# Kernel optimization log

Hardware: AMD Instinct MI355X
Metric: run time of the kernel (lower is better)

The kernel has to match this reference:

```python
import jax, jax.numpy as jnp
import numpy as np
import math

V, T, D_POI, D_OUT = 200000, 512, 256, 512
D_IN = D_POI + 4
D_HID = D_POI + 100


def setup_inputs() -> dict:
    key = jax.random.key(0)
    ks = jax.random.split(key, 12)
    s = 0.02
    return {
        "prev_poi_idx": jax.random.randint(ks[0], (T,), 0, V),
        "prev_time_frac": jax.random.uniform(ks[1], (T,), jnp.float32),
        "poi_final_emb": jax.random.normal(ks[2], (V, D_POI), jnp.float32),
        "poi_latlon_deg": jax.random.uniform(ks[3], (V, 2), jnp.float32) * 90.0,
        "ln_w": jnp.ones((D_IN,), jnp.float32),
        "ln_b": jnp.zeros((D_IN,), jnp.float32),
        "w1": jax.random.normal(ks[4], (D_IN, D_HID), jnp.float32) * s,
        "b1": jnp.zeros((D_HID,), jnp.float32),
        "w2": jax.random.normal(ks[5], (D_HID, D_POI), jnp.float32) * s,
        "b2": jnp.zeros((D_POI,), jnp.float32),
        "w_ih": jax.random.normal(ks[6], (3 * D_OUT, D_POI), jnp.float32) * s,
        "w_hh": jax.random.normal(ks[7], (3 * D_OUT, D_OUT), jnp.float32) * s,
        "b_ih": jnp.zeros((3 * D_OUT,), jnp.float32),
        "b_hh": jnp.zeros((3 * D_OUT,), jnp.float32),
        "q": jax.random.normal(ks[8], (D_OUT,), jnp.float32),
        "log_lam": jnp.array(0.0, jnp.float32),  # log(recency_lambda=1.0)
    }


def _haversine_km(lat1, lon1, lat2, lon2, eps=1e-12):
    dlat = (lat2 - lat1) * 0.5
    dlon = (lon2 - lon1) * 0.5
    a = jnp.sin(dlat) ** 2 + jnp.clip(jnp.cos(lat1), -1, 1) * jnp.clip(jnp.cos(lat2), -1, 1) * jnp.sin(dlon) ** 2
    c = 2.0 * jnp.arctan2(jnp.sqrt(jnp.clip(a, 0, 1)), jnp.sqrt(jnp.clip(1 - a, eps, 1)))
    return 6371.0088 * c


def _forward(prev_poi_idx, prev_time_frac, poi_final_emb, poi_latlon_deg,
             ln_w, ln_b, w1, b1, w2, b2, w_ih, w_hh, b_ih, b_hh, q, log_lam):
    Tn = prev_poi_idx.shape[0]
    poi_emb = poi_final_emb[prev_poi_idx]                       # (T, d_poi)
    t = jnp.clip(prev_time_frac, 0.0, 1.0)
    sin_t = jnp.sin(2.0 * math.pi * t)
    cos_t = jnp.cos(2.0 * math.pi * t)
    dif = jnp.mod(t[1:] - t[:-1], 1.0) * 24.0
    dt_h = jnp.concatenate([jnp.zeros((1,), t.dtype), dif])
    # _poi_radians is under no_grad in torch
    latlon = jax.lax.stop_gradient(poi_latlon_deg[prev_poi_idx])
    lat = jnp.deg2rad(jnp.clip(latlon[:, 0], -90, 90))
    lon = jnp.deg2rad(jnp.clip(latlon[:, 1], -180, 180))
    dd = _haversine_km(lat[:-1], lon[:-1], lat[1:], lon[1:])
    dd_km = jnp.concatenate([jnp.zeros((1,), dd.dtype), dd])
    feat = jnp.stack([sin_t, cos_t, jnp.log1p(dt_h), jnp.log1p(dd_km)], axis=-1)  # (T, 4)
    x = jnp.concatenate([poi_emb, feat], axis=-1)               # (T, d_poi+4)
    # fuse: LayerNorm -> Linear -> GELU -> (Dropout eval=id) -> Linear
    mu = jnp.mean(x, axis=-1, keepdims=True)
    var = jnp.mean((x - mu) ** 2, axis=-1, keepdims=True)
    x = (x - mu) * jax.lax.rsqrt(var + 1e-5) * ln_w + ln_b
    x = jax.nn.gelu(x @ w1 + b1, approximate=False) @ w2 + b2   # (T, d_poi)
    # GRU (single layer, unidirectional), torch gate order r,z,n
    gi_all = x @ w_ih.T + b_ih                                  # (T, 3H)
    def step(h, gi):
        gh = h @ w_hh.T + b_hh
        gi_r, gi_z, gi_n = jnp.split(gi, 3)
        gh_r, gh_z, gh_n = jnp.split(gh, 3)
        r = jax.nn.sigmoid(gi_r + gh_r)
        z = jax.nn.sigmoid(gi_z + gh_z)
        n = jnp.tanh(gi_n + r * gh_n)
        h_new = (1.0 - z) * n + z * h
        return h_new, h_new
    h0 = jnp.zeros((D_OUT,), x.dtype)
    _, hs = jax.lax.scan(step, h0, gi_all)                      # (T, d_out)
    D = hs.shape[-1]
    score = hs @ (q[:D] / jnp.sqrt(jnp.asarray(D, hs.dtype)))
    age = jnp.arange(Tn, dtype=hs.dtype)
    lam = jnp.maximum(jnp.exp(log_lam), 1e-4)
    score = score - lam * (Tn - 1 - age)
    attn = jax.nn.softmax(score, axis=0)
    summary = jnp.sum(attn[:, None] * hs, axis=0, keepdims=True)  # (1, d_out)
    return summary, attn


def reference(prev_poi_idx, prev_time_frac, poi_final_emb, poi_latlon_deg,
              ln_w, ln_b, w1, b1, w2, b2, w_ih, w_hh, b_ih, b_hh, q, log_lam):
    return _forward(prev_poi_idx, prev_time_frac, poi_final_emb, poi_latlon_deg,
                    ln_w, ln_b, w1, b1, w2, b2, w_ih, w_hh, b_ih, b_hh, q, log_lam)
```

## Files before the change

kernel.cpp:

```cpp
#include <hip/hip_runtime.h>
#include <hip/hip_cooperative_groups.h>
#include <math.h>

namespace cg = cooperative_groups;

#define TT 512
#define DPOI 256
#define DIN 260
#define DHID 356
#define DOUTD 512
#define G3 1536

#define GB 8
#define HU (DOUTD / GB)
#define NRR (3 * HU)
#define NPAY DOUTD

__global__ void ln_kernel(const int* __restrict__ idx, const float* __restrict__ timef,
                          const float* __restrict__ latlon, const float* __restrict__ emb,
                          const float* __restrict__ lnw, const float* __restrict__ lnb,
                          float* __restrict__ xn) {
    int t = blockIdx.x;
    int tid = threadIdx.x;
    int wave = tid >> 6, lane = tid & 63;

    float tv = fminf(fmaxf(timef[t], 0.f), 1.f);
    const float TWO_PI = 6.28318530717958647692f;
    float f0 = sinf(TWO_PI * tv);
    float f1 = cosf(TWO_PI * tv);
    float f2 = 0.f, f3 = 0.f;
    if (t > 0) {
        float tp = fminf(fmaxf(timef[t - 1], 0.f), 1.f);
        float d = tv - tp;
        d = d - floorf(d);
        f2 = log1pf(d * 24.f);
        int i0 = idx[t - 1], i1 = idx[t];
        float la0 = latlon[2 * (size_t)i0], lo0 = latlon[2 * (size_t)i0 + 1];
        float la1 = latlon[2 * (size_t)i1], lo1 = latlon[2 * (size_t)i1 + 1];
        const float D2R = 0.01745329251994329577f;
        float lat1 = fminf(fmaxf(la0, -90.f), 90.f) * D2R;
        float lon1 = fminf(fmaxf(lo0, -180.f), 180.f) * D2R;
        float lat2 = fminf(fmaxf(la1, -90.f), 90.f) * D2R;
        float lon2 = fminf(fmaxf(lo1, -180.f), 180.f) * D2R;
        float dlat = (lat2 - lat1) * 0.5f, dlon = (lon2 - lon1) * 0.5f;
        float sdlat = sinf(dlat), sdlon = sinf(dlon);
        float a = sdlat * sdlat +
                  fminf(fmaxf(cosf(lat1), -1.f), 1.f) * fminf(fmaxf(cosf(lat2), -1.f), 1.f) * sdlon * sdlon;
        float aa = fminf(fmaxf(a, 0.f), 1.f);
        float bb = fminf(fmaxf(1.f - a, 1e-12f), 1.f);
        float cc = 2.f * atan2f(sqrtf(aa), sqrtf(bb));
        f3 = log1pf(6371.0088f * cc);
    }
    float fv = (tid == 0) ? f0 : (tid == 1) ? f1 : (tid == 2) ? f2 : f3;

    const float* row = emb + (size_t)idx[t] * DPOI;
    float v0 = row[tid];
    float v1 = (tid < 4) ? fv : 0.f;

    __shared__ float red[4];
    __shared__ float mu_s, rs_s;

    float s = v0 + v1;
    for (int o = 32; o; o >>= 1) s += __shfl_down(s, o, 64);
    if (lane == 0) red[wave] = s;
    __syncthreads();
    if (tid == 0) mu_s = (red[0] + red[1] + red[2] + red[3]) * (1.f / 260.f);
    __syncthreads();
    float mu = mu_s;
    float d0 = v0 - mu;
    float d1 = (tid < 4) ? (v1 - mu) : 0.f;
    float sq = d0 * d0 + d1 * d1;
    for (int o = 32; o; o >>= 1) sq += __shfl_down(sq, o, 64);
    __syncthreads();
    if (lane == 0) red[wave] = sq;
    __syncthreads();
    if (tid == 0) {
        float var = (red[0] + red[1] + red[2] + red[3]) * (1.f / 260.f);
        rs_s = rsqrtf(var + 1e-5f);
    }
    __syncthreads();
    float rs = rs_s;
    xn[t * DIN + tid] = d0 * rs * lnw[tid] + lnb[tid];
    if (tid < 4)
        xn[t * DIN + 256 + tid] = d1 * rs * lnw[256 + tid] + lnb[256 + tid];
}

__global__ void mlp1_kernel(const float* __restrict__ xn, const float* __restrict__ w1,
                            const float* __restrict__ b1, float* __restrict__ h1) {
    int t = blockIdx.x, j = threadIdx.x;
    __shared__ float xl[DIN];
    for (int k = threadIdx.x; k < DIN; k += blockDim.x) xl[k] = xn[t * DIN + k];
    __syncthreads();
    if (j < DHID) {
        float acc = b1[j];
        #pragma unroll 4
        for (int k = 0; k < DIN; ++k) acc = fmaf(xl[k], w1[k * DHID + j], acc);
        float g = 0.5f * acc * (1.f + erff(acc * 0.70710678118654752440f));
        h1[t * DHID + j] = g;
    }
}

__global__ void mlp2_kernel(const float* __restrict__ h1, const float* __restrict__ w2,
                            const float* __restrict__ b2, float* __restrict__ x2) {
    int t = blockIdx.x, j = threadIdx.x;
    __shared__ float xl[DHID];
    for (int k = threadIdx.x; k < DHID; k += blockDim.x) xl[k] = h1[t * DHID + k];
    __syncthreads();
    float acc = b2[j];
    #pragma unroll 4
    for (int k = 0; k < DHID; ++k) acc = fmaf(xl[k], w2[k * DPOI + j], acc);
    x2[t * DPOI + j] = acc;
}

__global__ void gi_kernel(const float* __restrict__ x2, const float* __restrict__ wih,
                          const float* __restrict__ bih, float* __restrict__ gi,
                          uint4* __restrict__ hcz) {
    int t = blockIdx.x;
    int tid = threadIdx.x;
    int wave = tid >> 6, lane = tid & 63;
    uint4 z; z.x = 0u; z.y = 0u; z.z = 0u; z.w = 0u;
    hcz[(size_t)t * 256 + tid] = z;
    float4 xv = ((const float4*)(x2 + (size_t)t * DPOI))[lane];
    for (int r = wave; r < G3; r += 4) {
        float4 wv = ((const float4*)(wih + (size_t)r * DPOI))[lane];
        float s = xv.x * wv.x + xv.y * wv.y + xv.z * wv.z + xv.w * wv.w;
        for (int o = 32; o; o >>= 1) s += __shfl_down(s, o, 64);
        if (lane == 0) gi[(size_t)t * G3 + r] = s + bih[r];
    }
}

__global__ __launch_bounds__(1024)
void gru_fused_kernel(const float* __restrict__ gi, const float* __restrict__ whh,
                      const float* __restrict__ bhh, float* __restrict__ hs,
                      unsigned long long* __restrict__ hcomm,
                      const float* __restrict__ q, const float* __restrict__ log_lam,
                      float* __restrict__ out) {
    __shared__ float hprev[DOUTD];
    __shared__ float gsum[NRR];
    __shared__ float sc[TT];
    __shared__ float at[TT];
    __shared__ float red[8];
    __shared__ float red2[8];
    __shared__ float denom_s, mx_s;

    int b = blockIdx.x;
    int tid = threadIdx.x;
    int wave = tid >> 6, lane = tid & 63;
    int jbase = b * HU;
    int g4 = lane >> 4, l4 = lane & 15;
    int rr0 = wave * 12 + g4 * 3;

    float4 wf0[8], wf1[8], wf2[8];
    float bl0, bl1, bl2;
    {
        int r0 = rr0, r1 = rr0 + 1, r2 = rr0 + 2;
        const float4* p0 = (const float4*)(whh + (size_t)((r0 >> 6) * DOUTD + jbase + (r0 & 63)) * DOUTD);
        const float4* p1 = (const float4*)(whh + (size_t)((r1 >> 6) * DOUTD + jbase + (r1 & 63)) * DOUTD);
        const float4* p2 = (const float4*)(whh + (size_t)((r2 >> 6) * DOUTD + jbase + (r2 & 63)) * DOUTD);
        #pragma unroll
        for (int m = 0; m < 8; ++m) {
            wf0[m] = p0[m * 16 + l4];
            wf1[m] = p1[m * 16 + l4];
            wf2[m] = p2[m * 16 + l4];
        }
        bl0 = bhh[(r0 >> 6) * DOUTD + jbase + (r0 & 63)];
        bl1 = bhh[(r1 >> 6) * DOUTD + jbase + (r1 & 63)];
        bl2 = bhh[(r2 >> 6) * DOUTD + jbase + (r2 & 63)];
    }
    if (tid < DOUTD) hprev[tid] = 0.f;
    __syncthreads();

    const float4* hp4 = (const float4*)hprev;
    long budget = 2L * 1000 * 1000;
    float dj = (float)tid * 1e-6f;

    float gir = 0.f, giz = 0.f, gin = 0.f, hreg = 0.f;
    if (tid < HU) {
        int j = jbase + tid;
        gir = gi[j];
        giz = gi[DOUTD + j];
        gin = gi[2 * DOUTD + j];
    }

    for (int s = 0; s < TT; ++s) {
        if (s > 0) {
            if (tid >= 256 && tid < 768) {
                int u = tid - 256;
                bool own = (u >> 6) == b;
                const unsigned long long* ap = hcomm + (size_t)(s - 1) * NPAY + u;
                unsigned long long p = 0;
                bool ok = own;
                unsigned tagw = (unsigned)s;
                while (!__all(ok)) {
                    if (!ok) {
                        p = __hip_atomic_load(ap, __ATOMIC_RELAXED,
                                              __HIP_MEMORY_SCOPE_AGENT);
                        ok = ((unsigned)p == tagw);
                    }
                    float x = dj;
                    #pragma unroll
                    for (int zz = 0; zz < 8; ++zz) x = fmaf(x, 1.0000001f, 1e-7f);
                    dj = x;
                    if (--budget < 0) break;
                }
                if (!own) hprev[u] = __uint_as_float((unsigned)(p >> 32));
            }
            __syncthreads();
        }

        float a0 = 0.f, a1 = 0.f, a2 = 0.f;
        #pragma unroll
        for (int m = 0; m < 8; ++m) {
            float4 h4 = hp4[m * 16 + l4];
            a0 = fmaf(wf0[m].x, h4.x, a0); a0 = fmaf(wf0[m].y, h4.y, a0);
            a0 = fmaf(wf0[m].z, h4.z, a0); a0 = fmaf(wf0[m].w, h4.w, a0);
            a1 = fmaf(wf1[m].x, h4.x, a1); a1 = fmaf(wf1[m].y, h4.y, a1);
            a1 = fmaf(wf1[m].z, h4.z, a1); a1 = fmaf(wf1[m].w, h4.w, a1);
            a2 = fmaf(wf2[m].x, h4.x, a2); a2 = fmaf(wf2[m].y, h4.y, a2);
            a2 = fmaf(wf2[m].z, h4.z, a2); a2 = fmaf(wf2[m].w, h4.w, a2);
        }
        #pragma unroll
        for (int o = 1; o < 16; o <<= 1) {
            a0 += __shfl_xor(a0, o, 64);
            a1 += __shfl_xor(a1, o, 64);
            a2 += __shfl_xor(a2, o, 64);
        }
        if (l4 == 0) {
            gsum[rr0]     = a0 + bl0;
            gsum[rr0 + 1] = a1 + bl1;
            gsum[rr0 + 2] = a2 + bl2;
        }
        __syncthreads();

        if (tid < HU) {
            float gr  = gir + gsum[tid];
            float gz  = giz + gsum[HU + tid];
            float ghn = gsum[2 * HU + tid];
            float r = __builtin_amdgcn_rcpf(1.f + __expf(-gr));
            float z = __builtin_amdgcn_rcpf(1.f + __expf(-gz));
            float xt = gin + r * ghn;
            float n = 1.f - 2.f * __builtin_amdgcn_rcpf(__expf(2.f * xt) + 1.f);
            float hn = (1.f - z) * n + z * hreg;
            hreg = hn;
            unsigned ub = __float_as_uint(hn);
            ub += 0x7fffu + ((ub >> 16) & 1u);
            unsigned long long pay = ((unsigned long long)(ub & 0xffff0000u) << 32) |
                                     (unsigned)(s + 1);
            __hip_atomic_store(&hcomm[(size_t)s * NPAY + jbase + tid], pay,
                               __ATOMIC_RELAXED, __HIP_MEMORY_SCOPE_AGENT);
            int j = jbase + tid;
            hs[(size_t)s * DOUTD + j] = hn;
            hprev[j] = hn;
            if (s + 1 < TT) {
                const float* gn = gi + (size_t)(s + 1) * G3;
                gir = gn[j]; giz = gn[DOUTD + j]; gin = gn[2 * DOUTD + j];
            }
        }
    }

    asm volatile("" :: "v"(dj));

    cg::this_grid().sync();
    if (b != 0) return;

    const float qscale = 0.04419417382415921757f;
    for (int r = wave; r < TT; r += 16) {
        float acc = 0.f;
        #pragma unroll
        for (int m = 0; m < 8; ++m) {
            int k = lane + 64 * m;
            acc = fmaf(hs[(size_t)r * DOUTD + k], q[k], acc);
        }
        for (int o = 32; o; o >>= 1) acc += __shfl_down(acc, o, 64);
        if (lane == 0) sc[r] = acc * qscale;
    }
    __syncthreads();
    float lam = fmaxf(expf(log_lam[0]), 1e-4f);
    float s_i = (tid < TT) ? (sc[tid] - lam * (float)(TT - 1 - tid)) : -1e30f;

    float mval = s_i;
    for (int o = 32; o; o >>= 1) mval = fmaxf(mval, __shfl_down(mval, o, 64));
    if (lane == 0 && wave < 8) red[wave] = mval;
    __syncthreads();
    if (tid == 0) {
        float mm = red[0];
        for (int i = 1; i < 8; ++i) mm = fmaxf(mm, red[i]);
        mx_s = mm;
    }
    __syncthreads();
    float e = (tid < TT) ? expf(s_i - mx_s) : 0.f;
    float ssum = e;
    for (int o = 32; o; o >>= 1) ssum += __shfl_down(ssum, o, 64);
    if (lane == 0 && wave < 8) red2[wave] = ssum;
    __syncthreads();
    if (tid == 0) {
        float dsum = 0.f;
        for (int i = 0; i < 8; ++i) dsum += red2[i];
        denom_s = dsum;
    }
    __syncthreads();
    if (tid < TT) {
        float attn = e / denom_s;
        out[DOUTD + tid] = attn;
        at[tid] = attn;
    }
    __syncthreads();
    if (tid < TT) {
        float acc = 0.f;
        for (int i = 0; i < TT; ++i) acc = fmaf(at[i], hs[(size_t)i * DOUTD + tid], acc);
        out[tid] = acc;
    }
}

extern "C" void kernel_launch(void* const* d_in, const int* in_sizes, int n_in,
                              void* d_out, int out_size, void* d_ws, size_t ws_size,
                              hipStream_t stream) {
    const int*   idx    = (const int*)d_in[0];
    const float* timef  = (const float*)d_in[1];
    const float* emb    = (const float*)d_in[2];
    const float* latlon = (const float*)d_in[3];
    const float* lnw    = (const float*)d_in[4];
    const float* lnb    = (const float*)d_in[5];
    const float* w1     = (const float*)d_in[6];
    const float* b1     = (const float*)d_in[7];
    const float* w2     = (const float*)d_in[8];
    const float* b2     = (const float*)d_in[9];
    const float* wih    = (const float*)d_in[10];
    const float* whh    = (const float*)d_in[11];
    const float* bih    = (const float*)d_in[12];
    const float* bhh    = (const float*)d_in[13];
    const float* q      = (const float*)d_in[14];
    const float* loglam = (const float*)d_in[15];
    float* out = (float*)d_out;

    unsigned long long* hcomm = (unsigned long long*)d_ws;
    float* xn   = (float*)(hcomm + (size_t)TT * NPAY);
    float* h1   = xn + TT * DIN;
    float* x2   = h1 + TT * DHID;
    float* gi   = x2 + TT * DPOI;
    float* hs   = gi + (size_t)TT * G3;

    ln_kernel<<<TT, 256, 0, stream>>>(idx, timef, latlon, emb, lnw, lnb, xn);
    mlp1_kernel<<<TT, 384, 0, stream>>>(xn, w1, b1, h1);
    mlp2_kernel<<<TT, 256, 0, stream>>>(h1, w2, b2, x2);
    gi_kernel<<<TT, 256, 0, stream>>>(x2, wih, bih, gi, (uint4*)hcomm);

    void* gru_args[] = { (void*)&gi, (void*)&whh, (void*)&bhh, (void*)&hs,
                         (void*)&hcomm, (void*)&q, (void*)&loglam, (void*)&out };
    hipLaunchCooperativeKernel((void*)gru_fused_kernel, dim3(GB), dim3(1024),
                               gru_args, 0, stream);
}
```

Before: 1.849 ms.

## Fuse pre-GRU kernels, pack bf16 handoff into 32-bit words, split attention out

Merges the layernorm, two MLP layers and the input-gate projection into one kernel per timestep, with intermediates kept in shared memory, which removes three launches and their global round-trips. The GRU cross-block exchange now packs the bf16 hidden value and a 16-bit step tag into one 32-bit word. Waiting blocks poll it with hand-written inline assembly that keeps two loads in flight and uses a small retry budget. The cooperative launch and grid sync are replaced by ordinary launches plus a separate attention kernel. This relies on all 8 blocks being co-resident without a cooperative launch, and the short budget risks stale hidden values if a producer block lags.

```diff
diff --git a/kernel.cpp b/kernel.cpp
--- a/kernel.cpp
+++ b/kernel.cpp
@@ -1,8 +1,5 @@
 #include <hip/hip_runtime.h>
-#include <hip/hip_cooperative_groups.h>
 #include <math.h>
-
-namespace cg = cooperative_groups;
 
 #define TT 512
 #define DPOI 256
@@ -16,13 +13,25 @@
 #define NRR (3 * HU)
 #define NPAY DOUTD
 
-__global__ void ln_kernel(const int* __restrict__ idx, const float* __restrict__ timef,
-                          const float* __restrict__ latlon, const float* __restrict__ emb,
-                          const float* __restrict__ lnw, const float* __restrict__ lnb,
-                          float* __restrict__ xn) {
+__global__ __launch_bounds__(512)
+void pre_kernel(const int* __restrict__ idx, const float* __restrict__ timef,
+                const float* __restrict__ latlon, const float* __restrict__ emb,
+                const float* __restrict__ lnw, const float* __restrict__ lnb,
+                const float* __restrict__ w1, const float* __restrict__ b1,
+                const float* __restrict__ w2, const float* __restrict__ b2,
+                const float* __restrict__ wih, const float* __restrict__ bih,
+                float* __restrict__ gi, unsigned* __restrict__ hcz) {
     int t = blockIdx.x;
     int tid = threadIdx.x;
     int wave = tid >> 6, lane = tid & 63;
+
+    __shared__ float xl[DIN];
+    __shared__ float h1l[DHID];
+    __shared__ alignas(16) float x2l[DPOI];
+    __shared__ float red[8];
+    __shared__ float mu_s, rs_s;
+
+    hcz[(size_t)t * 512 + tid] = 0u;
 
     float tv = fminf(fmaxf(timef[t], 0.f), 1.f);
     const float TWO_PI = 6.28318530717958647692f;
@@ -53,21 +62,21 @@
     }
     float fv = (tid == 0) ? f0 : (tid == 1) ? f1 : (tid == 2) ? f2 : f3;
 
-    const float* row = emb + (size_t)idx[t] * DPOI;
-    float v0 = row[tid];
+    float v0 = (tid < 256) ? emb[(size_t)idx[t] * DPOI + tid] : 0.f;
     float v1 = (tid < 4) ? fv : 0.f;
-
-    __shared__ float red[4];
-    __shared__ float mu_s, rs_s;
 
     float s = v0 + v1;
     for (int o = 32; o; o >>= 1) s += __shfl_down(s, o, 64);
     if (lane == 0) red[wave] = s;
     __syncthreads();
-    if (tid == 0) mu_s = (red[0] + red[1] + red[2] + red[3]) * (1.f / 260.f);
+    if (tid == 0) {
+        float mm = 0.f;
+        for (int i = 0; i < 8; ++i) mm += red[i];
+        mu_s = mm * (1.f / 260.f);
+    }
     __syncthreads();
     float mu = mu_s;
-    float d0 = v0 - mu;
+    float d0 = (tid < 256) ? (v0 - mu) : 0.f;
     float d1 = (tid < 4) ? (v1 - mu) : 0.f;
     float sq = d0 * d0 + d1 * d1;
     for (int o = 32; o; o >>= 1) sq += __shfl_down(sq, o, 64);
@@ -75,73 +84,47 @@
     if (lane == 0) red[wave] = sq;
     __syncthreads();
     if (tid == 0) {
-        float var = (red[0] + red[1] + red[2] + red[3]) * (1.f / 260.f);
-        rs_s = rsqrtf(var + 1e-5f);
+        float vv = 0.f;
+        for (int i = 0; i < 8; ++i) vv += red[i];
+        rs_s = rsqrtf(vv * (1.f / 260.f) + 1e-5f);
     }
     __syncthreads();
     float rs = rs_s;
-    xn[t * DIN + tid] = d0 * rs * lnw[tid] + lnb[tid];
-    if (tid < 4)
-        xn[t * DIN + 256 + tid] = d1 * rs * lnw[256 + tid] + lnb[256 + tid];
+    if (tid < 256) xl[tid] = d0 * rs * lnw[tid] + lnb[tid];
+    if (tid < 4)   xl[256 + tid] = d1 * rs * lnw[256 + tid] + lnb[256 + tid];
+    __syncthreads();
+
+    if (tid < DHID) {
+        float acc = b1[tid];
+        #pragma unroll 4
+        for (int k = 0; k < DIN; ++k) acc = fmaf(xl[k], w1[k * DHID + tid], acc);
+        h1l[tid] = 0.5f * acc * (1.f + erff(acc * 0.70710678118654752440f));
+    }
+    __syncthreads();
+
+    if (tid < DPOI) {
+        float acc = b2[tid];
+        #pragma unroll 4
+        for (int k = 0; k < DHID; ++k) acc = fmaf(h1l[k], w2[k * DPOI + tid], acc);
+        x2l[tid] = acc;
+    }
+    __syncthreads();
+
+    float4 xv = ((const float4*)x2l)[lane];
+    for (int r = wave; r < G3; r += 8) {
+        float4 wv = ((const float4*)(wih + (size_t)r * DPOI))[lane];
+        float sd = xv.x * wv.x + xv.y * wv.y + xv.z * wv.z + xv.w * wv.w;
+        for (int o = 32; o; o >>= 1) sd += __shfl_down(sd, o, 64);
+        if (lane == 0) gi[(size_t)t * G3 + r] = sd + bih[r];
+    }
 }
 
-__global__ void mlp1_kernel(const float* __restrict__ xn, const float* __restrict__ w1,
-                            const float* __restrict__ b1, float* __restrict__ h1) {
-    int t = blockIdx.x, j = threadIdx.x;
-    __shared__ float xl[DIN];
-    for (int k = threadIdx.x; k < DIN; k += blockDim.x) xl[k] = xn[t * DIN + k];
-    __syncthreads();
-    if (j < DHID) {
-        float acc = b1[j];
-        #pragma unroll 4
-        for (int k = 0; k < DIN; ++k) acc = fmaf(xl[k], w1[k * DHID + j], acc);
-        float g = 0.5f * acc * (1.f + erff(acc * 0.70710678118654752440f));
-        h1[t * DHID + j] = g;
-    }
-}
-
-__global__ void mlp2_kernel(const float* __restrict__ h1, const float* __restrict__ w2,
-                            const float* __restrict__ b2, float* __restrict__ x2) {
-    int t = blockIdx.x, j = threadIdx.x;
-    __shared__ float xl[DHID];
-    for (int k = threadIdx.x; k < DHID; k += blockDim.x) xl[k] = h1[t * DHID + k];
-    __syncthreads();
-    float acc = b2[j];
-    #pragma unroll 4
-    for (int k = 0; k < DHID; ++k) acc = fmaf(xl[k], w2[k * DPOI + j], acc);
-    x2[t * DPOI + j] = acc;
-}
-
-__global__ void gi_kernel(const float* __restrict__ x2, const float* __restrict__ wih,
-                          const float* __restrict__ bih, float* __restrict__ gi,
-                          uint4* __restrict__ hcz) {
-    int t = blockIdx.x;
-    int tid = threadIdx.x;
-    int wave = tid >> 6, lane = tid & 63;
-    uint4 z; z.x = 0u; z.y = 0u; z.z = 0u; z.w = 0u;
-    hcz[(size_t)t * 256 + tid] = z;
-    float4 xv = ((const float4*)(x2 + (size_t)t * DPOI))[lane];
-    for (int r = wave; r < G3; r += 4) {
-        float4 wv = ((const float4*)(wih + (size_t)r * DPOI))[lane];
-        float s = xv.x * wv.x + xv.y * wv.y + xv.z * wv.z + xv.w * wv.w;
-        for (int o = 32; o; o >>= 1) s += __shfl_down(s, o, 64);
-        if (lane == 0) gi[(size_t)t * G3 + r] = s + bih[r];
-    }
-}
-
 __global__ __launch_bounds__(1024)
-void gru_fused_kernel(const float* __restrict__ gi, const float* __restrict__ whh,
-                      const float* __restrict__ bhh, float* __restrict__ hs,
-                      unsigned long long* __restrict__ hcomm,
-                      const float* __restrict__ q, const float* __restrict__ log_lam,
-                      float* __restrict__ out) {
-    __shared__ float hprev[DOUTD];
+void gru_kernel(const float* __restrict__ gi, const float* __restrict__ whh,
+                const float* __restrict__ bhh, float* __restrict__ hs,
+                unsigned* __restrict__ hcomm) {
+    __shared__ alignas(16) float hprev[DOUTD];
     __shared__ float gsum[NRR];
-    __shared__ float sc[TT];
-    __shared__ float at[TT];
-    __shared__ float red[8];
-    __shared__ float red2[8];
-    __shared__ float denom_s, mx_s;
 
     int b = blockIdx.x;
     int tid = threadIdx.x;
@@ -171,8 +154,7 @@
     __syncthreads();
 
     const float4* hp4 = (const float4*)hprev;
-    long budget = 2L * 1000 * 1000;
-    float dj = (float)tid * 1e-6f;
+    long budget = 3000;
 
     float gir = 0.f, giz = 0.f, gin = 0.f, hreg = 0.f;
     if (tid < HU) {
@@ -183,29 +165,50 @@
     }
 
     for (int s = 0; s < TT; ++s) {
+        unsigned pa = 0, pb = 0;
         if (s > 0) {
-            if (tid >= 256 && tid < 768) {
-                int u = tid - 256;
-                bool own = (u >> 6) == b;
-                const unsigned long long* ap = hcomm + (size_t)(s - 1) * NPAY + u;
-                unsigned long long p = 0;
-                bool ok = own;
-                unsigned tagw = (unsigned)s;
-                while (!__all(ok)) {
-                    if (!ok) {
-                        p = __hip_atomic_load(ap, __ATOMIC_RELAXED,
-                                              __HIP_MEMORY_SCOPE_AGENT);
-                        ok = ((unsigned)p == tagw);
-                    }
-                    float x = dj;
-                    #pragma unroll
-                    for (int zz = 0; zz < 8; ++zz) x = fmaf(x, 1.0000001f, 1e-7f);
-                    dj = x;
-                    if (--budget < 0) break;
-                }
-                if (!own) hprev[u] = __uint_as_float((unsigned)(p >> 32));
+            if (wave >= 4 && wave < 12 && (wave - 4) != b) {
+                int u = ((wave - 4) << 6) + lane;
+                const unsigned* ap = hcomm + (size_t)(s - 1) * NPAY + u;
+                unsigned tag = (unsigned)s & 0xffffu;
+                asm volatile("global_load_dword %0, %1, off sc0 sc1"
+                             : "=v"(pa) : "v"(ap) : "memory");
+                float xx = (float)(lane + 1) * 1e-6f;
+                #pragma unroll
+                for (int q = 0; q < 256; ++q) xx = fmaf(xx, 1.0000002f, 1.1920929e-7f);
+                asm volatile("global_load_dword %0, %1, off sc0 sc1"
+                             : "=v"(pb) : "v"(ap), "v"(xx) : "memory");
+                do {
+                    unsigned tmp; int scnt;
+                    asm volatile(
+                        "s_movk_i32 %[cnt], 64\n\t"
+                        "1:\n\t"
+                        "s_waitcnt vmcnt(1)\n\t"
+                        "v_and_b32 %[t], 0xffff, %[pa]\n\t"
+                        "v_cmp_ne_u32 vcc, %[tag], %[t]\n\t"
+                        "s_cbranch_vccz 9f\n\t"
+                        "global_load_dword %[pa], %[ptr], off sc0 sc1\n\t"
+                        "s_waitcnt vmcnt(1)\n\t"
+                        "v_and_b32 %[t], 0xffff, %[pb]\n\t"
+                        "v_cmp_ne_u32 vcc, %[tag], %[t]\n\t"
+                        "s_cbranch_vccz 8f\n\t"
+                        "global_load_dword %[pb], %[ptr], off sc0 sc1\n\t"
+                        "s_sub_u32 %[cnt], %[cnt], 1\n\t"
+                        "s_cmp_lg_u32 %[cnt], 0\n\t"
+                        "s_cbranch_scc1 1b\n\t"
+                        "s_branch 9f\n\t"
+                        "8:\n\t"
+                        "v_mov_b32 %[pa], %[pb]\n\t"
+                        "9:\n\t"
+                        : [pa]"+v"(pa), [pb]"+v"(pb), [t]"=&v"(tmp), [cnt]"=&s"(scnt)
+                        : [ptr]"v"(ap), [tag]"s"(tag)
+                        : "vcc", "scc", "memory");
+                    if ((pa & 0xffffu) == tag) break;
+                } while (--budget > 0);
+                hprev[u] = __uint_as_float(pa & 0xffff0000u);
             }
             __syncthreads();
+            asm volatile("" :: "v"(pa), "v"(pb));
         }
 
         float a0 = 0.f, a1 = 0.f, a2 = 0.f;
@@ -244,8 +247,7 @@
             hreg = hn;
             unsigned ub = __float_as_uint(hn);
             ub += 0x7fffu + ((ub >> 16) & 1u);
-            unsigned long long pay = ((unsigned long long)(ub & 0xffff0000u) << 32) |
-                                     (unsigned)(s + 1);
+            unsigned pay = (ub & 0xffff0000u) | ((unsigned)(s + 1) & 0xffffu);
             __hip_atomic_store(&hcomm[(size_t)s * NPAY + jbase + tid], pay,
                                __ATOMIC_RELAXED, __HIP_MEMORY_SCOPE_AGENT);
             int j = jbase + tid;
@@ -257,14 +259,20 @@
             }
         }
     }
-
-    asm volatile("" :: "v"(dj));
-
-    cg::this_grid().sync();
-    if (b != 0) return;
+}
+
+__global__ void attn_kernel(const float* __restrict__ hs, const float* __restrict__ q,
+                            const float* __restrict__ log_lam, float* __restrict__ out) {
+    int tid = threadIdx.x;
+    int wave = tid >> 6, lane = tid & 63;
+    __shared__ float sc[TT];
+    __shared__ float at[TT];
+    __shared__ float red[8];
+    __shared__ float red2[8];
+    __shared__ float denom_s, mx_s;
 
     const float qscale = 0.04419417382415921757f;
-    for (int r = wave; r < TT; r += 16) {
+    for (int r = wave; r < TT; r += 8) {
         float acc = 0.f;
         #pragma unroll
         for (int m = 0; m < 8; ++m) {
@@ -276,11 +284,11 @@
     }
     __syncthreads();
     float lam = fmaxf(expf(log_lam[0]), 1e-4f);
-    float s_i = (tid < TT) ? (sc[tid] - lam * (float)(TT - 1 - tid)) : -1e30f;
+    float s_i = sc[tid] - lam * (float)(TT - 1 - tid);
 
     float mval = s_i;
     for (int o = 32; o; o >>= 1) mval = fmaxf(mval, __shfl_down(mval, o, 64));
-    if (lane == 0 && wave < 8) red[wave] = mval;
+    if (lane == 0) red[wave] = mval;
     __syncthreads();
     if (tid == 0) {
         float mm = red[0];
@@ -288,10 +296,10 @@
         mx_s = mm;
     }
     __syncthreads();
-    float e = (tid < TT) ? expf(s_i - mx_s) : 0.f;
+    float e = expf(s_i - mx_s);
     float ssum = e;
     for (int o = 32; o; o >>= 1) ssum += __shfl_down(ssum, o, 64);
-    if (lane == 0 && wave < 8) red2[wave] = ssum;
+    if (lane == 0) red2[wave] = ssum;
     __syncthreads();
     if (tid == 0) {
         float dsum = 0.f;
@@ -299,17 +307,13 @@
         denom_s = dsum;
     }
     __syncthreads();
-    if (tid < TT) {
-        float attn = e / denom_s;
-        out[DOUTD + tid] = attn;
-        at[tid] = attn;
-    }
-    __syncthreads();
-    if (tid < TT) {
-        float acc = 0.f;
-        for (int i = 0; i < TT; ++i) acc = fmaf(at[i], hs[(size_t)i * DOUTD + tid], acc);
-        out[tid] = acc;
-    }
+    float attn = e / denom_s;
+    out[DOUTD + tid] = attn;
+    at[tid] = attn;
+    __syncthreads();
+    float acc = 0.f;
+    for (int i = 0; i < TT; ++i) acc = fmaf(at[i], hs[(size_t)i * DOUTD + tid], acc);
+    out[tid] = acc;
 }
 
 extern "C" void kernel_launch(void* const* d_in, const int* in_sizes, int n_in,
@@ -333,20 +337,12 @@
     const float* loglam = (const float*)d_in[15];
     float* out = (float*)d_out;
 
-    unsigned long long* hcomm = (unsigned long long*)d_ws;
-    float* xn   = (float*)(hcomm + (size_t)TT * NPAY);
-    float* h1   = xn + TT * DIN;
-    float* x2   = h1 + TT * DHID;
-    float* gi   = x2 + TT * DPOI;
-    float* hs   = gi + (size_t)TT * G3;
-
-    ln_kernel<<<TT, 256, 0, stream>>>(idx, timef, latlon, emb, lnw, lnb, xn);
-    mlp1_kernel<<<TT, 384, 0, stream>>>(xn, w1, b1, h1);
-    mlp2_kernel<<<TT, 256, 0, stream>>>(h1, w2, b2, x2);
-    gi_kernel<<<TT, 256, 0, stream>>>(x2, wih, bih, gi, (uint4*)hcomm);
-
-    void* gru_args[] = { (void*)&gi, (void*)&whh, (void*)&bhh, (void*)&hs,
-                         (void*)&hcomm, (void*)&q, (void*)&loglam, (void*)&out };
-    hipLaunchCooperativeKernel((void*)gru_fused_kernel, dim3(GB), dim3(1024),
-                               gru_args, 0, stream);
+    unsigned* hcomm = (unsigned*)d_ws;
+    float* gi = (float*)(hcomm + (size_t)TT * NPAY);
+    float* hs = gi + (size_t)TT * G3;
+
+    pre_kernel<<<TT, 512, 0, stream>>>(idx, timef, latlon, emb, lnw, lnb,
+                                       w1, b1, w2, b2, wih, bih, gi, hcomm);
+    gru_kernel<<<GB, 1024, 0, stream>>>(gi, whh, bhh, hs, hcomm);
+    attn_kernel<<<1, TT, 0, stream>>>(hs, q, loglam, out);
 }
```

Result: faster. 1.536 ms (-16.9%).
